# Kernel tuning notes

Hardware: AMD Instinct MI355X
Metric: run time of the kernel (lower is better)

Reference implementation:

```python
import jax, jax.numpy as jnp
import numpy as np

B, NF, QUERY_DIM = 4, 300, 512
HIDDEN, NUM_HEADS = 512, 8
H, W = 80, 80
HEAD_DIM = HIDDEN // NUM_HEADS
NORM_FACT = float(HIDDEN / NUM_HEADS) ** (-0.5)


def setup_inputs() -> dict:
    key = jax.random.key(0)
    k1, k2, k3, k4, k5 = jax.random.split(key, 5)
    # xavier_uniform bound for [HIDDEN, QUERY_DIM] weight
    bound = float(np.sqrt(6.0 / (HIDDEN + QUERY_DIM)))
    return {
        "q": jax.random.normal(k1, (B, NF, QUERY_DIM), dtype=jnp.float32),
        "k": jax.random.normal(k2, (B, QUERY_DIM, H, W), dtype=jnp.float32),
        "mask": jax.random.bernoulli(k3, 0.25, (B, H, W)),  # True = masked out
        "q_w": jax.random.uniform(k4, (HIDDEN, QUERY_DIM), jnp.float32, -bound, bound),
        "q_b": jnp.zeros((HIDDEN,), jnp.float32),
        "k_w": jax.random.uniform(k5, (HIDDEN, QUERY_DIM), jnp.float32, -bound, bound),
        "k_b": jnp.zeros((HIDDEN,), jnp.float32),
    }


def reference(q, k, mask, q_w, q_b, k_w, k_b):
    b, nf, _ = q.shape
    h, w = k.shape[-2], k.shape[-1]
    # q projection: [b, nf, hidden]
    qp = jnp.einsum("bqd,ed->bqe", q, q_w) + q_b
    # k projection (1x1 conv == channel matmul): [b, hidden, h, w]
    kp = jnp.einsum("bdhw,ed->behw", k, k_w) + k_b[None, :, None, None]
    # split heads
    qh = qp.reshape(b, nf, NUM_HEADS, HEAD_DIM) * NORM_FACT   # [b,q,n,c]
    kh = kp.reshape(b, NUM_HEADS, HEAD_DIM, h, w)             # [b,n,c,h,w]
    # batched QK scores (replaces the per-query python loop + cat(dim=2))
    weights = jnp.einsum("bqnc,bnchw->bqnhw", qh, kh)
    weights = weights.reshape(b, 1, nf * NUM_HEADS, h, w)
    # masked_fill with -inf on padded spatial positions
    weights = jnp.where(mask[:, None, None, :, :], -jnp.inf, weights)
    # NOTE: softmax over flatten(2) = jointly over (queries*heads*h*w), as in source
    weights = jax.nn.softmax(weights.reshape(b, 1, -1), axis=-1)
    return weights.reshape(b, 1, nf * NUM_HEADS, h, w)
```

## Files before the change

kernel.cpp:

```cpp
#include <hip/hip_runtime.h>
#include <math.h>

#define B_    4
#define NF    300
#define QD    512
#define HID   512
#define NH    8
#define HD    64
#define HW    6400
#define ROWS  2400
#define NQP   384
#define NORM_FACT 0.125f
#define NEG_INF (-INFINITY)
#define LDK   40

typedef __bf16 bf16_t;
typedef __bf16 bf16x4_t __attribute__((ext_vector_type(4)));
typedef __bf16 bf16x8_t __attribute__((ext_vector_type(8)));
typedef float  f32x4    __attribute__((ext_vector_type(4)));

__device__ __forceinline__ void splitf(float x, bf16_t& h, bf16_t& l) {
    h = (bf16_t)x;
    l = (bf16_t)(x - (float)h);
}
__device__ __forceinline__ int swz(int c, int row) {
    return (((c >> 3) ^ (row & 7)) << 3) | (c & 7);
}

__global__ __launch_bounds__(256) void qproj_kernel(
    const float* __restrict__ q, const float* __restrict__ qw,
    const float* __restrict__ qb, bf16_t* __restrict__ qh_hi,
    bf16_t* __restrict__ qh_lo)
{
    __shared__ float qs[4][QD];
    const int r0    = blockIdx.x * 4;
    const int b     = r0 / NF;
    const int qbase = r0 % NF;
    const int t     = threadIdx.x;
    #pragma unroll
    for (int row = 0; row < 4; ++row) {
        qs[row][t]       = q[(size_t)(r0 + row) * QD + t];
        qs[row][t + 256] = q[(size_t)(r0 + row) * QD + t + 256];
    }
    __syncthreads();
    #pragma unroll
    for (int eo = 0; eo < 2; ++eo) {
        const int e = t + eo * 256;
        const int n = e >> 6, c = e & 63;
        float a[4] = {0.f, 0.f, 0.f, 0.f};
        for (int d = 0; d < QD; d += 4) {
            float4 w = *(const float4*)&qw[(size_t)e * QD + d];
            #pragma unroll
            for (int row = 0; row < 4; ++row)
                a[row] += qs[row][d]*w.x + qs[row][d+1]*w.y
                        + qs[row][d+2]*w.z + qs[row][d+3]*w.w;
        }
        const float bias = qb[e];
        #pragma unroll
        for (int row = 0; row < 4; ++row) {
            const int qq = qbase + row;
            const float val = (a[row] + bias) * NORM_FACT;
            bf16_t h, l; splitf(val, h, l);
            size_t off = ((size_t)(b * NH + n) * NQP + qq) * 64 + swz(c, qq);
            qh_hi[off] = h; qh_lo[off] = l;
        }
    }
}

__global__ __launch_bounds__(256) void kproj_mfma(
    const float* __restrict__ k, const float* __restrict__ kw,
    const float* __restrict__ kb, bf16_t* __restrict__ kp_hi,
    bf16_t* __restrict__ kp_lo)
{
    __shared__ __align__(16) bf16_t Ah[128][LDK];
    __shared__ __align__(16) bf16_t Al[128][LDK];
    __shared__ __align__(16) bf16_t Bh[128][LDK];
    __shared__ __align__(16) bf16_t Bl[128][LDK];
    const int b  = blockIdx.z;
    const int e0 = blockIdx.y * 128;
    const int p0 = blockIdx.x * 128;
    const int t  = threadIdx.x;
    const int wave = t >> 6, lane = t & 63;
    const int wr = wave >> 1, wc = wave & 1;
    const int lm = lane & 15, lq = lane >> 4;
    const float* kB = k + (size_t)b * QD * HW;

    f32x4 acc[4][4];
    const f32x4 zero4 = {0.f, 0.f, 0.f, 0.f};
    #pragma unroll
    for (int i = 0; i < 4; ++i)
        #pragma unroll
        for (int j = 0; j < 4; ++j) acc[i][j] = zero4;

    for (int d0 = 0; d0 < QD; d0 += 32) {
        #pragma unroll
        for (int i = 0; i < 4; ++i) {
            int idx = t + i * 256;
            int p = idx & 127, db = (idx >> 7) << 2;
            bf16x4_t hv, lv;
            #pragma unroll
            for (int j = 0; j < 4; ++j) {
                float x = kB[(size_t)(d0 + db + j) * HW + p0 + p];
                bf16_t hx, lx; splitf(x, hx, lx);
                hv[j] = hx; lv[j] = lx;
            }
            *(bf16x4_t*)&Ah[p][db] = hv;
            *(bf16x4_t*)&Al[p][db] = lv;
        }
        #pragma unroll
        for (int i = 0; i < 4; ++i) {
            int idx = t + i * 256;
            int e = idx >> 3, dp = (idx & 7) << 2;
            float4 v = *(const float4*)&kw[(size_t)(e0 + e) * QD + d0 + dp];
            bf16x4_t hv, lv; bf16_t hx, lx;
            splitf(v.x, hx, lx); hv[0] = hx; lv[0] = lx;
            splitf(v.y, hx, lx); hv[1] = hx; lv[1] = lx;
            splitf(v.z, hx, lx); hv[2] = hx; lv[2] = lx;
            splitf(v.w, hx, lx); hv[3] = hx; lv[3] = lx;
            *(bf16x4_t*)&Bh[e][dp] = hv;
            *(bf16x4_t*)&Bl[e][dp] = lv;
        }
        __syncthreads();

        bf16x8_t ah[4], al[4], bh[4], bl[4];
        #pragma unroll
        for (int mt = 0; mt < 4; ++mt) {
            int r = wr * 64 + mt * 16 + lm;
            ah[mt] = *(const bf16x8_t*)&Ah[r][lq * 8];
            al[mt] = *(const bf16x8_t*)&Al[r][lq * 8];
        }
        #pragma unroll
        for (int nt = 0; nt < 4; ++nt) {
            int c = wc * 64 + nt * 16 + lm;
            bh[nt] = *(const bf16x8_t*)&Bh[c][lq * 8];
            bl[nt] = *(const bf16x8_t*)&Bl[c][lq * 8];
        }
        #pragma unroll
        for (int mt = 0; mt < 4; ++mt)
            #pragma unroll
            for (int nt = 0; nt < 4; ++nt) {
                f32x4 a = acc[mt][nt];
                a = __builtin_amdgcn_mfma_f32_16x16x32_bf16(al[mt], bh[nt], a, 0, 0, 0);
                a = __builtin_amdgcn_mfma_f32_16x16x32_bf16(ah[mt], bl[nt], a, 0, 0, 0);
                a = __builtin_amdgcn_mfma_f32_16x16x32_bf16(ah[mt], bh[nt], a, 0, 0, 0);
                acc[mt][nt] = a;
            }
        __syncthreads();
    }

    #pragma unroll
    for (int nt = 0; nt < 4; ++nt) {
        const int e = e0 + wc * 64 + nt * 16 + lm;
        const int n = e >> 6;
        const int c = (nt * 16 + lm) & 63;
        const float bias = kb[e];
        bf16_t* dh = kp_hi + (size_t)(b * NH + n) * HW * 64;
        bf16_t* dl = kp_lo + (size_t)(b * NH + n) * HW * 64;
        #pragma unroll
        for (int mt = 0; mt < 4; ++mt) {
            #pragma unroll
            for (int reg = 0; reg < 4; ++reg) {
                int p = p0 + wr * 64 + mt * 16 + lq * 4 + reg;
                float val = acc[mt][nt][reg] + bias;
                bf16_t h, l; splitf(val, h, l);
                size_t off = (size_t)p * 64 + swz(c, p);
                dh[off] = h; dl[off] = l;
            }
        }
    }
}

__global__ __launch_bounds__(256) void scores_pass_a(
    const bf16_t* __restrict__ qh_hi, const bf16_t* __restrict__ kp_hi,
    const int* __restrict__ mask, float* __restrict__ partials)
{
    __shared__ __align__(16) bf16_t At[128 * 64];
    __shared__ __align__(16) bf16_t Bt[128 * 64];
    __shared__ float redM[256];
    __shared__ float redS[256];
    const int z  = blockIdx.z;
    const int b  = z >> 3, n = z & 7;
    const int q0 = blockIdx.y * 128;
    const int p0 = blockIdx.x * 128;
    const int t  = threadIdx.x;
    const int wave = t >> 6, lane = t & 63;
    const int wr = wave >> 1, wc = wave & 1;
    const int lm = lane & 15, lq = lane >> 4;

    const uint4* ga = (const uint4*)(qh_hi + ((size_t)(b * NH + n) * NQP + q0) * 64);
    const uint4* gb = (const uint4*)(kp_hi + ((size_t)(b * NH + n) * HW  + p0) * 64);
    uint4* la = (uint4*)At;
    uint4* lb = (uint4*)Bt;
    #pragma unroll
    for (int i = 0; i < 4; ++i) {
        la[t + i * 256] = ga[t + i * 256];
        lb[t + i * 256] = gb[t + i * 256];
    }
    __syncthreads();

    f32x4 acc[4][4];
    const f32x4 zero4 = {0.f, 0.f, 0.f, 0.f};
    #pragma unroll
    for (int i = 0; i < 4; ++i)
        #pragma unroll
        for (int j = 0; j < 4; ++j) acc[i][j] = zero4;

    #pragma unroll
    for (int ks = 0; ks < 2; ++ks) {
        bf16x8_t af[4], bf[4];
        #pragma unroll
        for (int mt = 0; mt < 4; ++mt) {
            int row = wr * 64 + mt * 16 + lm;
            af[mt] = *(const bf16x8_t*)&At[row * 64 + (((lq + ks * 4) ^ (lm & 7)) << 3)];
        }
        #pragma unroll
        for (int nt = 0; nt < 4; ++nt) {
            int row = wc * 64 + nt * 16 + lm;
            bf[nt] = *(const bf16x8_t*)&Bt[row * 64 + (((lq + ks * 4) ^ (lm & 7)) << 3)];
        }
        #pragma unroll
        for (int mt = 0; mt < 4; ++mt)
            #pragma unroll
            for (int nt = 0; nt < 4; ++nt)
                acc[mt][nt] = __builtin_amdgcn_mfma_f32_16x16x32_bf16(
                    af[mt], bf[nt], acc[mt][nt], 0, 0, 0);
    }

    int mm[4];
    #pragma unroll
    for (int nt = 0; nt < 4; ++nt)
        mm[nt] = mask[b * HW + p0 + wc * 64 + nt * 16 + lm];

    float tm = NEG_INF;
    #pragma unroll
    for (int mt = 0; mt < 4; ++mt) {
        int qbase = q0 + wr * 64 + mt * 16 + lq * 4;
        #pragma unroll
        for (int reg = 0; reg < 4; ++reg) {
            if (qbase + reg < NF) {
                #pragma unroll
                for (int nt = 0; nt < 4; ++nt)
                    if (!mm[nt]) tm = fmaxf(tm, acc[mt][nt][reg]);
            }
        }
    }
    float ts = 0.f;
    if (tm != NEG_INF) {
        #pragma unroll
        for (int mt = 0; mt < 4; ++mt) {
            int qbase = q0 + wr * 64 + mt * 16 + lq * 4;
            #pragma unroll
            for (int reg = 0; reg < 4; ++reg) {
                if (qbase + reg < NF) {
                    #pragma unroll
                    for (int nt = 0; nt < 4; ++nt)
                        if (!mm[nt]) ts += __expf(acc[mt][nt][reg] - tm);
                }
            }
        }
    }

    redM[t] = tm; redS[t] = ts;
    __syncthreads();
    for (int off = 128; off > 0; off >>= 1) {
        if (t < off) {
            float m1 = redM[t],       s1 = redS[t];
            float m2 = redM[t + off], s2 = redS[t + off];
            float M = fmaxf(m1, m2);
            float s = (M == NEG_INF) ? 0.f
                      : (s1 * __expf(m1 - M) + s2 * __expf(m2 - M));
            redM[t] = M; redS[t] = s;
        }
        __syncthreads();
    }
    if (t == 0) {
        int lin = (z * gridDim.y + blockIdx.y) * gridDim.x + blockIdx.x;
        partials[2 * lin]     = redM[0];
        partials[2 * lin + 1] = redS[0];
    }
}

__global__ __launch_bounds__(256) void stats_kernel(
    const float* __restrict__ partials, float* __restrict__ stats, int nper)
{
    __shared__ float redM[256];
    __shared__ float redS[256];
    const int b = blockIdx.x, t = threadIdx.x;
    const float* p = partials + (size_t)b * nper * 2;
    float m = NEG_INF, s = 0.f;
    for (int i = t; i < nper; i += 256) {
        float m2 = p[2 * i], s2 = p[2 * i + 1];
        float M = fmaxf(m, m2);
        float ns = (M == NEG_INF) ? 0.f
                   : (s * __expf(m - M) + s2 * __expf(m2 - M));
        m = M; s = ns;
    }
    redM[t] = m; redS[t] = s;
    __syncthreads();
    for (int off = 128; off > 0; off >>= 1) {
        if (t < off) {
            float m1 = redM[t],       s1 = redS[t];
            float m2 = redM[t + off], s2 = redS[t + off];
            float M = fmaxf(m1, m2);
            float ns = (M == NEG_INF) ? 0.f
                       : (s1 * __expf(m1 - M) + s2 * __expf(m2 - M));
            redM[t] = M; redS[t] = ns;
        }
        __syncthreads();
    }
    if (t == 0) {
        stats[2 * b]     = redM[0];
        stats[2 * b + 1] = 1.0f / redS[0];
    }
}

__global__ __launch_bounds__(256) void scores_pass_b(
    const bf16_t* __restrict__ qh_hi, const bf16_t* __restrict__ qh_lo,
    const bf16_t* __restrict__ kp_hi, const bf16_t* __restrict__ kp_lo,
    const int* __restrict__ mask, const float* __restrict__ stats,
    float* __restrict__ out)
{
    __shared__ __align__(16) bf16_t Aht[128 * 64];
    __shared__ __align__(16) bf16_t Alt[128 * 64];
    __shared__ __align__(16) bf16_t Bht[128 * 64];
    __shared__ __align__(16) bf16_t Blt[128 * 64];
    const int z  = blockIdx.z;
    const int b  = z >> 3, n = z & 7;
    const int q0 = blockIdx.y * 128;
    const int p0 = blockIdx.x * 128;
    const int t  = threadIdx.x;
    const int wave = t >> 6, lane = t & 63;
    const int wr = wave >> 1, wc = wave & 1;
    const int lm = lane & 15, lq = lane >> 4;

    const float M    = stats[2 * b];
    const float invS = stats[2 * b + 1];

    const size_t abase = ((size_t)(b * NH + n) * NQP + q0) * 64;
    const size_t bbase = ((size_t)(b * NH + n) * HW  + p0) * 64;
    const uint4* gah = (const uint4*)(qh_hi + abase);
    const uint4* gal = (const uint4*)(qh_lo + abase);
    const uint4* gbh = (const uint4*)(kp_hi + bbase);
    const uint4* gbl = (const uint4*)(kp_lo + bbase);
    #pragma unroll
    for (int i = 0; i < 4; ++i) {
        ((uint4*)Aht)[t + i * 256] = gah[t + i * 256];
        ((uint4*)Alt)[t + i * 256] = gal[t + i * 256];
        ((uint4*)Bht)[t + i * 256] = gbh[t + i * 256];
        ((uint4*)Blt)[t + i * 256] = gbl[t + i * 256];
    }
    __syncthreads();

    f32x4 acc[4][4];
    const f32x4 zero4 = {0.f, 0.f, 0.f, 0.f};
    #pragma unroll
    for (int i = 0; i < 4; ++i)
        #pragma unroll
        for (int j = 0; j < 4; ++j) acc[i][j] = zero4;

    #pragma unroll
    for (int ks = 0; ks < 2; ++ks) {
        bf16x8_t ah[4], al[4], bh[4], bl[4];
        #pragma unroll
        for (int mt = 0; mt < 4; ++mt) {
            int row = wr * 64 + mt * 16 + lm;
            int off = row * 64 + (((lq + ks * 4) ^ (lm & 7)) << 3);
            ah[mt] = *(const bf16x8_t*)&Aht[off];
            al[mt] = *(const bf16x8_t*)&Alt[off];
        }
        #pragma unroll
        for (int nt = 0; nt < 4; ++nt) {
            int row = wc * 64 + nt * 16 + lm;
            int off = row * 64 + (((lq + ks * 4) ^ (lm & 7)) << 3);
            bh[nt] = *(const bf16x8_t*)&Bht[off];
            bl[nt] = *(const bf16x8_t*)&Blt[off];
        }
        #pragma unroll
        for (int mt = 0; mt < 4; ++mt)
            #pragma unroll
            for (int nt = 0; nt < 4; ++nt) {
                f32x4 a = acc[mt][nt];
                a = __builtin_amdgcn_mfma_f32_16x16x32_bf16(al[mt], bh[nt], a, 0, 0, 0);
                a = __builtin_amdgcn_mfma_f32_16x16x32_bf16(ah[mt], bl[nt], a, 0, 0, 0);
                a = __builtin_amdgcn_mfma_f32_16x16x32_bf16(ah[mt], bh[nt], a, 0, 0, 0);
                acc[mt][nt] = a;
            }
    }

    int mm[4];
    #pragma unroll
    for (int nt = 0; nt < 4; ++nt)
        mm[nt] = mask[b * HW + p0 + wc * 64 + nt * 16 + lm];

    #pragma unroll
    for (int mt = 0; mt < 4; ++mt) {
        #pragma unroll
        for (int reg = 0; reg < 4; ++reg) {
            int qg = q0 + wr * 64 + mt * 16 + lq * 4 + reg;
            if (qg < NF) {
                float* dst = out + (size_t)(b * ROWS + qg * NH + n) * HW + p0 + wc * 64 + lm;
                #pragma unroll
                for (int nt = 0; nt < 4; ++nt)
                    dst[nt * 16] = mm[nt] ? 0.f : __expf(acc[mt][nt][reg] - M) * invS;
            }
        }
    }
}

extern "C" void kernel_launch(void* const* d_in, const int* in_sizes, int n_in,
                              void* d_out, int out_size, void* d_ws, size_t ws_size,
                              hipStream_t stream) {
    const float* q    = (const float*)d_in[0];
    const float* k    = (const float*)d_in[1];
    const int*   mask = (const int*)  d_in[2];
    const float* qw   = (const float*)d_in[3];
    const float* qb   = (const float*)d_in[4];
    const float* kw   = (const float*)d_in[5];
    const float* kb   = (const float*)d_in[6];
    float* out = (float*)d_out;

    bf16_t* kp_hi = (bf16_t*)d_ws;
    bf16_t* kp_lo = kp_hi + (size_t)B_ * NH * HW * 64;
    bf16_t* qh_hi = kp_lo + (size_t)B_ * NH * HW * 64;
    bf16_t* qh_lo = qh_hi + (size_t)B_ * NH * NQP * 64;
    float* partials = (float*)(qh_lo + (size_t)B_ * NH * NQP * 64);
    float* stats    = partials + 2 * 4800;

    qproj_kernel<<<300, 256, 0, stream>>>(q, qw, qb, qh_hi, qh_lo);
    kproj_mfma<<<dim3(50, 4, 4), 256, 0, stream>>>(k, kw, kb, kp_hi, kp_lo);
    scores_pass_a<<<dim3(50, 3, 32), 256, 0, stream>>>(qh_hi, kp_hi, mask, partials);
    stats_kernel<<<4, 256, 0, stream>>>(partials, stats, 1200);
    scores_pass_b<<<dim3(50, 3, 32), 256, 0, stream>>>(qh_hi, qh_lo, kp_hi, kp_lo,
                                                       mask, stats, out);
}
```

Baseline: 498.8 us.

## Merge projection kernels, stream Q fragments from global, vectorize output stores

The q and k projections are merged into one launch that dispatches on block index, so the two can run concurrently. In both score passes, Q fragments are now loaded straight from global into registers instead of being staged in LDS. This halves LDS use and adds occupancy hints, and waves whose query tile is entirely padding skip their work. Operands are swapped so each lane owns four consecutive spatial positions, which allows int4 mask loads and 16-byte nontemporal float4 output stores in place of scalar strided stores.

```diff
diff --git a/kernel.cpp b/kernel.cpp
--- a/kernel.cpp
+++ b/kernel.cpp
@@ -27,13 +27,13 @@
     return (((c >> 3) ^ (row & 7)) << 3) | (c & 7);
 }
 
-__global__ __launch_bounds__(256) void qproj_kernel(
-    const float* __restrict__ q, const float* __restrict__ qw,
-    const float* __restrict__ qb, bf16_t* __restrict__ qh_hi,
-    bf16_t* __restrict__ qh_lo)
-{
-    __shared__ float qs[4][QD];
-    const int r0    = blockIdx.x * 4;
+__device__ __forceinline__ void qproj_body(
+    char* smem, int blk, const float* __restrict__ q,
+    const float* __restrict__ qw, const float* __restrict__ qb,
+    bf16_t* __restrict__ qh_hi, bf16_t* __restrict__ qh_lo)
+{
+    float (*qs)[QD] = (float (*)[QD])smem;
+    const int r0    = blk * 4;
     const int b     = r0 / NF;
     const int qbase = r0 % NF;
     const int t     = threadIdx.x;
@@ -67,18 +67,17 @@
     }
 }
 
-__global__ __launch_bounds__(256) void kproj_mfma(
-    const float* __restrict__ k, const float* __restrict__ kw,
-    const float* __restrict__ kb, bf16_t* __restrict__ kp_hi,
-    bf16_t* __restrict__ kp_lo)
-{
-    __shared__ __align__(16) bf16_t Ah[128][LDK];
-    __shared__ __align__(16) bf16_t Al[128][LDK];
-    __shared__ __align__(16) bf16_t Bh[128][LDK];
-    __shared__ __align__(16) bf16_t Bl[128][LDK];
-    const int b  = blockIdx.z;
-    const int e0 = blockIdx.y * 128;
-    const int p0 = blockIdx.x * 128;
+__device__ __forceinline__ void kproj_body(
+    char* smem, int px, int ey, int b, const float* __restrict__ k,
+    const float* __restrict__ kw, const float* __restrict__ kb,
+    bf16_t* __restrict__ kp_hi, bf16_t* __restrict__ kp_lo)
+{
+    bf16_t (*Ah)[LDK] = (bf16_t (*)[LDK])(smem);
+    bf16_t (*Al)[LDK] = (bf16_t (*)[LDK])(smem + 10240);
+    bf16_t (*Bh)[LDK] = (bf16_t (*)[LDK])(smem + 20480);
+    bf16_t (*Bl)[LDK] = (bf16_t (*)[LDK])(smem + 30720);
+    const int e0 = ey * 128;
+    const int p0 = px * 128;
     const int t  = threadIdx.x;
     const int wave = t >> 6, lane = t & 63;
     const int wr = wave >> 1, wc = wave & 1;
@@ -170,12 +169,79 @@
     }
 }
 
-__global__ __launch_bounds__(256) void scores_pass_a(
+__global__ __launch_bounds__(256) void proj_kernel(
+    const float* __restrict__ q, const float* __restrict__ qw,
+    const float* __restrict__ qb, const float* __restrict__ k,
+    const float* __restrict__ kw, const float* __restrict__ kb,
+    bf16_t* __restrict__ qh_hi, bf16_t* __restrict__ qh_lo,
+    bf16_t* __restrict__ kp_hi, bf16_t* __restrict__ kp_lo)
+{
+    __shared__ __align__(16) char smem[40960];
+    const int bx = blockIdx.x;
+    if (bx < 800) {
+        kproj_body(smem, bx % 50, (bx / 50) % 4, bx / 200, k, kw, kb, kp_hi, kp_lo);
+    } else {
+        qproj_body(smem, bx - 800, q, qw, qb, qh_hi, qh_lo);
+    }
+}
+
+template<int KS>
+__device__ __forceinline__ void load_qf(const bf16_t* __restrict__ qp,
+                                        int lm, int lq, bf16x8_t (&f)[4])
+{
+    #pragma unroll
+    for (int nt = 0; nt < 4; ++nt) {
+        const size_t o = (size_t)(nt * 16 + lm) * 64
+                       + (size_t)((((KS * 4 + lq) ^ (lm & 7))) << 3);
+        f[nt] = *(const bf16x8_t*)(qp + o);
+    }
+}
+
+template<int KS>
+__device__ __forceinline__ void ks_mfma_hi(const bf16_t* Kh, int wr, int lm, int lq,
+                                           const bf16x8_t (&qh)[4], f32x4 (&acc)[4][4])
+{
+    #pragma unroll
+    for (int mt = 0; mt < 4; ++mt) {
+        const int row = wr * 64 + mt * 16 + lm;
+        const int off = row * 64 + ((((KS * 4 + lq) ^ (lm & 7))) << 3);
+        const bf16x8_t ah = *(const bf16x8_t*)&Kh[off];
+        #pragma unroll
+        for (int nt = 0; nt < 4; ++nt)
+            acc[mt][nt] = __builtin_amdgcn_mfma_f32_16x16x32_bf16(
+                ah, qh[nt], acc[mt][nt], 0, 0, 0);
+    }
+}
+
+template<int KS>
+__device__ __forceinline__ void ks_mfma_split(const bf16_t* Kh, const bf16_t* Kl,
+                                              int wr, int lm, int lq,
+                                              const bf16x8_t (&qh)[4],
+                                              const bf16x8_t (&ql)[4],
+                                              f32x4 (&acc)[4][4])
+{
+    #pragma unroll
+    for (int mt = 0; mt < 4; ++mt) {
+        const int row = wr * 64 + mt * 16 + lm;
+        const int off = row * 64 + ((((KS * 4 + lq) ^ (lm & 7))) << 3);
+        const bf16x8_t ah = *(const bf16x8_t*)&Kh[off];
+        const bf16x8_t al = *(const bf16x8_t*)&Kl[off];
+        #pragma unroll
+        for (int nt = 0; nt < 4; ++nt) {
+            f32x4 a = acc[mt][nt];
+            a = __builtin_amdgcn_mfma_f32_16x16x32_bf16(al, qh[nt], a, 0, 0, 0);
+            a = __builtin_amdgcn_mfma_f32_16x16x32_bf16(ah, ql[nt], a, 0, 0, 0);
+            a = __builtin_amdgcn_mfma_f32_16x16x32_bf16(ah, qh[nt], a, 0, 0, 0);
+            acc[mt][nt] = a;
+        }
+    }
+}
+
+__global__ __launch_bounds__(256, 4) void scores_pass_a(
     const bf16_t* __restrict__ qh_hi, const bf16_t* __restrict__ kp_hi,
     const int* __restrict__ mask, float* __restrict__ partials)
 {
-    __shared__ __align__(16) bf16_t At[128 * 64];
-    __shared__ __align__(16) bf16_t Bt[128 * 64];
+    __shared__ __align__(16) bf16_t Kh[128 * 64];
     __shared__ float redM[256];
     __shared__ float redS[256];
     const int z  = blockIdx.z;
@@ -186,75 +252,58 @@
     const int wave = t >> 6, lane = t & 63;
     const int wr = wave >> 1, wc = wave & 1;
     const int lm = lane & 15, lq = lane >> 4;
-
-    const uint4* ga = (const uint4*)(qh_hi + ((size_t)(b * NH + n) * NQP + q0) * 64);
-    const uint4* gb = (const uint4*)(kp_hi + ((size_t)(b * NH + n) * HW  + p0) * 64);
-    uint4* la = (uint4*)At;
-    uint4* lb = (uint4*)Bt;
-    #pragma unroll
-    for (int i = 0; i < 4; ++i) {
-        la[t + i * 256] = ga[t + i * 256];
-        lb[t + i * 256] = gb[t + i * 256];
-    }
+    const bool wave_active = (q0 + wc * 64) < NF;
+
+    const uint4* gb = (const uint4*)(kp_hi + ((size_t)(b * NH + n) * HW + p0) * 64);
+    uint4* lb = (uint4*)Kh;
+    #pragma unroll
+    for (int i = 0; i < 4; ++i) lb[t + i * 256] = gb[t + i * 256];
+
+    const bf16_t* qph = qh_hi + ((size_t)(b * NH + n) * NQP + q0 + wc * 64) * 64;
+    bf16x8_t qf0[4];
+    if (wave_active) load_qf<0>(qph, lm, lq, qf0);
     __syncthreads();
 
-    f32x4 acc[4][4];
-    const f32x4 zero4 = {0.f, 0.f, 0.f, 0.f};
-    #pragma unroll
-    for (int i = 0; i < 4; ++i)
-        #pragma unroll
-        for (int j = 0; j < 4; ++j) acc[i][j] = zero4;
-
-    #pragma unroll
-    for (int ks = 0; ks < 2; ++ks) {
-        bf16x8_t af[4], bf[4];
-        #pragma unroll
-        for (int mt = 0; mt < 4; ++mt) {
-            int row = wr * 64 + mt * 16 + lm;
-            af[mt] = *(const bf16x8_t*)&At[row * 64 + (((lq + ks * 4) ^ (lm & 7)) << 3)];
-        }
+    float tm = NEG_INF, ts = 0.f;
+    if (wave_active) {
+        f32x4 acc[4][4];
+        const f32x4 zero4 = {0.f, 0.f, 0.f, 0.f};
+        #pragma unroll
+        for (int i = 0; i < 4; ++i)
+            #pragma unroll
+            for (int j = 0; j < 4; ++j) acc[i][j] = zero4;
+
+        bf16x8_t qf1[4];
+        load_qf<1>(qph, lm, lq, qf1);
+        ks_mfma_hi<0>(Kh, wr, lm, lq, qf0, acc);
+        ks_mfma_hi<1>(Kh, wr, lm, lq, qf1, acc);
+
+        int4 mm4[4];
+        #pragma unroll
+        for (int mt = 0; mt < 4; ++mt)
+            mm4[mt] = *(const int4*)&mask[b * HW + p0 + wr * 64 + mt * 16 + lq * 4];
+
         #pragma unroll
         for (int nt = 0; nt < 4; ++nt) {
-            int row = wc * 64 + nt * 16 + lm;
-            bf[nt] = *(const bf16x8_t*)&Bt[row * 64 + (((lq + ks * 4) ^ (lm & 7)) << 3)];
-        }
-        #pragma unroll
-        for (int mt = 0; mt < 4; ++mt)
-            #pragma unroll
-            for (int nt = 0; nt < 4; ++nt)
-                acc[mt][nt] = __builtin_amdgcn_mfma_f32_16x16x32_bf16(
-                    af[mt], bf[nt], acc[mt][nt], 0, 0, 0);
-    }
-
-    int mm[4];
-    #pragma unroll
-    for (int nt = 0; nt < 4; ++nt)
-        mm[nt] = mask[b * HW + p0 + wc * 64 + nt * 16 + lm];
-
-    float tm = NEG_INF;
-    #pragma unroll
-    for (int mt = 0; mt < 4; ++mt) {
-        int qbase = q0 + wr * 64 + mt * 16 + lq * 4;
-        #pragma unroll
-        for (int reg = 0; reg < 4; ++reg) {
-            if (qbase + reg < NF) {
+            if (q0 + wc * 64 + nt * 16 + lm < NF) {
                 #pragma unroll
-                for (int nt = 0; nt < 4; ++nt)
-                    if (!mm[nt]) tm = fmaxf(tm, acc[mt][nt][reg]);
-            }
-        }
-    }
-    float ts = 0.f;
-    if (tm != NEG_INF) {
-        #pragma unroll
-        for (int mt = 0; mt < 4; ++mt) {
-            int qbase = q0 + wr * 64 + mt * 16 + lq * 4;
-            #pragma unroll
-            for (int reg = 0; reg < 4; ++reg) {
-                if (qbase + reg < NF) {
+                for (int mt = 0; mt < 4; ++mt)
                     #pragma unroll
-                    for (int nt = 0; nt < 4; ++nt)
-                        if (!mm[nt]) ts += __expf(acc[mt][nt][reg] - tm);
+                    for (int reg = 0; reg < 4; ++reg)
+                        if (!((const int*)&mm4[mt])[reg])
+                            tm = fmaxf(tm, acc[mt][nt][reg]);
+            }
+        }
+        if (tm != NEG_INF) {
+            #pragma unroll
+            for (int nt = 0; nt < 4; ++nt) {
+                if (q0 + wc * 64 + nt * 16 + lm < NF) {
+                    #pragma unroll
+                    for (int mt = 0; mt < 4; ++mt)
+                        #pragma unroll
+                        for (int reg = 0; reg < 4; ++reg)
+                            if (!((const int*)&mm4[mt])[reg])
+                                ts += __expf(acc[mt][nt][reg] - tm);
                 }
             }
         }
@@ -314,16 +363,14 @@
     }
 }
 
-__global__ __launch_bounds__(256) void scores_pass_b(
+__global__ __launch_bounds__(256, 3) void scores_pass_b(
     const bf16_t* __restrict__ qh_hi, const bf16_t* __restrict__ qh_lo,
     const bf16_t* __restrict__ kp_hi, const bf16_t* __restrict__ kp_lo,
     const int* __restrict__ mask, const float* __restrict__ stats,
     float* __restrict__ out)
 {
-    __shared__ __align__(16) bf16_t Aht[128 * 64];
-    __shared__ __align__(16) bf16_t Alt[128 * 64];
-    __shared__ __align__(16) bf16_t Bht[128 * 64];
-    __shared__ __align__(16) bf16_t Blt[128 * 64];
+    __shared__ __align__(16) bf16_t Kh[128 * 64];
+    __shared__ __align__(16) bf16_t Kl[128 * 64];
     const int z  = blockIdx.z;
     const int b  = z >> 3, n = z & 7;
     const int q0 = blockIdx.y * 128;
@@ -332,24 +379,30 @@
     const int wave = t >> 6, lane = t & 63;
     const int wr = wave >> 1, wc = wave & 1;
     const int lm = lane & 15, lq = lane >> 4;
+    const bool wave_active = (q0 + wc * 64) < NF;
 
     const float M    = stats[2 * b];
     const float invS = stats[2 * b + 1];
 
-    const size_t abase = ((size_t)(b * NH + n) * NQP + q0) * 64;
-    const size_t bbase = ((size_t)(b * NH + n) * HW  + p0) * 64;
-    const uint4* gah = (const uint4*)(qh_hi + abase);
-    const uint4* gal = (const uint4*)(qh_lo + abase);
+    const size_t bbase = ((size_t)(b * NH + n) * HW + p0) * 64;
     const uint4* gbh = (const uint4*)(kp_hi + bbase);
     const uint4* gbl = (const uint4*)(kp_lo + bbase);
     #pragma unroll
     for (int i = 0; i < 4; ++i) {
-        ((uint4*)Aht)[t + i * 256] = gah[t + i * 256];
-        ((uint4*)Alt)[t + i * 256] = gal[t + i * 256];
-        ((uint4*)Bht)[t + i * 256] = gbh[t + i * 256];
-        ((uint4*)Blt)[t + i * 256] = gbl[t + i * 256];
+        ((uint4*)Kh)[t + i * 256] = gbh[t + i * 256];
+        ((uint4*)Kl)[t + i * 256] = gbl[t + i * 256];
+    }
+
+    const size_t qoff = ((size_t)(b * NH + n) * NQP + q0 + wc * 64) * 64;
+    const bf16_t* qph = qh_hi + qoff;
+    const bf16_t* qpl = qh_lo + qoff;
+    bf16x8_t qh0[4], ql0[4];
+    if (wave_active) {
+        load_qf<0>(qph, lm, lq, qh0);
+        load_qf<0>(qpl, lm, lq, ql0);
     }
     __syncthreads();
+    if (!wave_active) return;
 
     f32x4 acc[4][4];
     const f32x4 zero4 = {0.f, 0.f, 0.f, 0.f};
@@ -358,50 +411,31 @@
         #pragma unroll
         for (int j = 0; j < 4; ++j) acc[i][j] = zero4;
 
-    #pragma unroll
-    for (int ks = 0; ks < 2; ++ks) {
-        bf16x8_t ah[4], al[4], bh[4], bl[4];
-        #pragma unroll
-        for (int mt = 0; mt < 4; ++mt) {
-            int row = wr * 64 + mt * 16 + lm;
-            int off = row * 64 + (((lq + ks * 4) ^ (lm & 7)) << 3);
-            ah[mt] = *(const bf16x8_t*)&Aht[off];
-            al[mt] = *(const bf16x8_t*)&Alt[off];
-        }
-        #pragma unroll
-        for (int nt = 0; nt < 4; ++nt) {
-            int row = wc * 64 + nt * 16 + lm;
-            int off = row * 64 + (((lq + ks * 4) ^ (lm & 7)) << 3);
-            bh[nt] = *(const bf16x8_t*)&Bht[off];
-            bl[nt] = *(const bf16x8_t*)&Blt[off];
-        }
-        #pragma unroll
-        for (int mt = 0; mt < 4; ++mt)
-            #pragma unroll
-            for (int nt = 0; nt < 4; ++nt) {
-                f32x4 a = acc[mt][nt];
-                a = __builtin_amdgcn_mfma_f32_16x16x32_bf16(al[mt], bh[nt], a, 0, 0, 0);
-                a = __builtin_amdgcn_mfma_f32_16x16x32_bf16(ah[mt], bl[nt], a, 0, 0, 0);
-                a = __builtin_amdgcn_mfma_f32_16x16x32_bf16(ah[mt], bh[nt], a, 0, 0, 0);
-                acc[mt][nt] = a;
-            }
-    }
-
-    int mm[4];
-    #pragma unroll
-    for (int nt = 0; nt < 4; ++nt)
-        mm[nt] = mask[b * HW + p0 + wc * 64 + nt * 16 + lm];
-
-    #pragma unroll
-    for (int mt = 0; mt < 4; ++mt) {
-        #pragma unroll
-        for (int reg = 0; reg < 4; ++reg) {
-            int qg = q0 + wr * 64 + mt * 16 + lq * 4 + reg;
-            if (qg < NF) {
-                float* dst = out + (size_t)(b * ROWS + qg * NH + n) * HW + p0 + wc * 64 + lm;
+    bf16x8_t qh1[4], ql1[4];
+    load_qf<1>(qph, lm, lq, qh1);
+    load_qf<1>(qpl, lm, lq, ql1);
+    ks_mfma_split<0>(Kh, Kl, wr, lm, lq, qh0, ql0, acc);
+    ks_mfma_split<1>(Kh, Kl, wr, lm, lq, qh1, ql1, acc);
+
+    int4 mm4[4];
+    #pragma unroll
+    for (int mt = 0; mt < 4; ++mt)
+        mm4[mt] = *(const int4*)&mask[b * HW + p0 + wr * 64 + mt * 16 + lq * 4];
+
+    #pragma unroll
+    for (int nt = 0; nt < 4; ++nt) {
+        const int qg = q0 + wc * 64 + nt * 16 + lm;
+        if (qg < NF) {
+            float* rowp = out + (size_t)(b * ROWS + qg * NH + n) * HW + p0 + wr * 64;
+            #pragma unroll
+            for (int mt = 0; mt < 4; ++mt) {
+                f32x4 v;
                 #pragma unroll
-                for (int nt = 0; nt < 4; ++nt)
-                    dst[nt * 16] = mm[nt] ? 0.f : __expf(acc[mt][nt][reg] - M) * invS;
+                for (int reg = 0; reg < 4; ++reg) {
+                    const int msk = ((const int*)&mm4[mt])[reg];
+                    v[reg] = msk ? 0.f : __expf(acc[mt][nt][reg] - M) * invS;
+                }
+                __builtin_nontemporal_store(v, (f32x4*)(rowp + mt * 16 + lq * 4));
             }
         }
     }
@@ -426,8 +460,8 @@
     float* partials = (float*)(qh_lo + (size_t)B_ * NH * NQP * 64);
     float* stats    = partials + 2 * 4800;
 
-    qproj_kernel<<<300, 256, 0, stream>>>(q, qw, qb, qh_hi, qh_lo);
-    kproj_mfma<<<dim3(50, 4, 4), 256, 0, stream>>>(k, kw, kb, kp_hi, kp_lo);
+    proj_kernel<<<1100, 256, 0, stream>>>(q, qw, qb, k, kw, kb,
+                                          qh_hi, qh_lo, kp_hi, kp_lo);
     scores_pass_a<<<dim3(50, 3, 32), 256, 0, stream>>>(qh_hi, kp_hi, mask, partials);
     stats_kernel<<<4, 256, 0, stream>>>(partials, stats, 1200);
     scores_pass_b<<<dim3(50, 3, 32), 256, 0, stream>>>(qh_hi, qh_lo, kp_hi, kp_lo,
```

After: 477.0 us, median of 2. -4.4%, faster.
